# Optimization experiments

Hardware: AMD Instinct MI355X
Metric: run time of the kernel (lower is better)

## Reference

```python
import jax, jax.numpy as jnp
import numpy as np

EPS = 1e-5

def _ln(x, g, b):
    mu = jnp.mean(x, axis=-1, keepdims=True)
    var = jnp.mean((x - mu) ** 2, axis=-1, keepdims=True)
    return (x - mu) * jax.lax.rsqrt(var + EPS) * g + b

def setup_inputs() -> dict:
    key = jax.random.key(0)
    B, V, I, H = 32, 48, 24, 768
    ks = jax.random.split(key, 10)
    s = 0.02
    return {
        'variables': jax.random.normal(ks[0], (B, V, H), jnp.float32),
        'interventions': jax.random.normal(ks[1], (B, I, H), jnp.float32),
        # variable_encoder: Linear(H,H) + LayerNorm(H)
        'W_enc': jax.random.normal(ks[2], (H, H), jnp.float32) * s,
        'b_enc': jnp.zeros((H,), jnp.float32),
        'g_enc': jnp.ones((H,), jnp.float32),
        'be_enc': jnp.zeros((H,), jnp.float32),
        # graph_generator: Linear(2H,H) + LN(H) + ReLU + Linear(H,1) + Sigmoid
        'Wg1': jax.random.normal(ks[3], (2 * H, H), jnp.float32) * s,
        'bg1': jnp.zeros((H,), jnp.float32),
        'g_g': jnp.ones((H,), jnp.float32),
        'b_g': jnp.zeros((H,), jnp.float32),
        'Wg2': jax.random.normal(ks[4], (H, 1), jnp.float32) * s,
        'bg2': jnp.zeros((1,), jnp.float32),
        # intervention_predictor: Linear(2H,H) + LN(H) + ReLU + Linear(H,H)
        'Wi1': jax.random.normal(ks[5], (2 * H, H), jnp.float32) * s,
        'bi1': jnp.zeros((H,), jnp.float32),
        'g_i': jnp.ones((H,), jnp.float32),
        'b_i': jnp.zeros((H,), jnp.float32),
        'Wi2': jax.random.normal(ks[6], (H, H), jnp.float32) * s,
        'bi2': jnp.zeros((H,), jnp.float32),
    }

def reference(variables, interventions, W_enc, b_enc, g_enc, be_enc,
              Wg1, bg1, g_g, b_g, Wg2, bg2, Wi1, bi1, g_i, b_i, Wi2, bi2):
    H = variables.shape[-1]
    V = variables.shape[1]
    # variable encoder: Linear + LayerNorm + ReLU
    enc = jax.nn.relu(_ln(variables @ W_enc + b_enc, g_enc, be_enc))  # [B,V,H]

    # graph generator over all ordered pairs (i,j): concat([enc_i, enc_j]) @ Wg1
    # split Wg1 so the concat-matmul becomes two small GEMMs + broadcast add
    hi = jnp.einsum('bvh,hk->bvk', enc, Wg1[:H])   # contribution of enc_i
    hj = jnp.einsum('bvh,hk->bvk', enc, Wg1[H:])   # contribution of enc_j
    h = jax.nn.relu(_ln(hi[:, :, None, :] + hj[:, None, :, :] + bg1, g_g, b_g))  # [B,V,V,H]
    score = jax.nn.sigmoid(jnp.squeeze(h @ Wg2, -1) + bg2[0])  # [B,V,V]
    # diagonal (i==j) is never written in the original -> stays zero
    causal_graph = score * (1.0 - jnp.eye(V, dtype=score.dtype))

    # intervention predictor: concat([intervention_i, enc_j]) -> MLP
    ha = jnp.einsum('bih,hk->bik', interventions, Wi1[:H])  # [B,I,H]
    hb = jnp.einsum('bvh,hk->bvk', enc, Wi1[H:])            # [B,V,H]
    h2 = jax.nn.relu(_ln(ha[:, :, None, :] + hb[:, None, :, :] + bi1, g_i, b_i))  # [B,I,V,H]
    effects = h2 @ Wi2 + bi2  # [B,I,V,H]

    return (effects, causal_graph, enc)
```

## Files before the change

### kernel.cpp

```cpp
#include <hip/hip_runtime.h>
#include <math.h>

#define Bp 32
#define Vp 48
#define Ip 24
#define Hp 768
#define EPS 1e-5f

#define EFFECTS_SIZE (Bp*Ip*Vp*Hp)
#define GRAPH_SIZE   (Bp*Vp*Vp)
#define ENC_SIZE     (Bp*Vp*Hp)
#define MS           (Hp*Hp)

typedef __attribute__((ext_vector_type(8))) short short8;
typedef __attribute__((ext_vector_type(4))) float floatx4;
typedef __attribute__((ext_vector_type(2))) float floatx2;
typedef __attribute__((ext_vector_type(2))) unsigned int uintx2;
typedef __attribute__((ext_vector_type(4))) unsigned int uintx4;

__device__ __forceinline__ unsigned short f2bf(float f) {
    unsigned int u = __float_as_uint(f);
    u += 0x7fffu + ((u >> 16) & 1u);
    return (unsigned short)(u >> 16);
}
__device__ __forceinline__ unsigned int f2bf2(float a, float b) {
    return (unsigned int)f2bf(a) | ((unsigned int)f2bf(b) << 16);
}

__device__ __forceinline__ uintx4 ln8(floatx4 xa, floatx4 xb, float mu, float rs,
                                      floatx4 ga, floatx4 gb, floatx4 ba, floatx4 bb)
{
    float y0 = fmaxf((xa.x - mu) * rs * ga.x + ba.x, 0.f);
    float y1 = fmaxf((xa.y - mu) * rs * ga.y + ba.y, 0.f);
    float y2 = fmaxf((xa.z - mu) * rs * ga.z + ba.z, 0.f);
    float y3 = fmaxf((xa.w - mu) * rs * ga.w + ba.w, 0.f);
    float y4 = fmaxf((xb.x - mu) * rs * gb.x + bb.x, 0.f);
    float y5 = fmaxf((xb.y - mu) * rs * gb.y + bb.y, 0.f);
    float y6 = fmaxf((xb.z - mu) * rs * gb.z + bb.z, 0.f);
    float y7 = fmaxf((xb.w - mu) * rs * gb.w + bb.w, 0.f);
    uintx4 v;
    v.x = f2bf2(y0, y1); v.y = f2bf2(y2, y3);
    v.z = f2bf2(y4, y5); v.w = f2bf2(y6, y7);
    return v;
}

__global__ __launch_bounds__(256) void pack_weights(
    const float* __restrict__ W_enc, const float* __restrict__ Wg1,
    const float* __restrict__ Wi1, const float* __restrict__ Wi2,
    unsigned short* __restrict__ packed)
{
    const int bid = blockIdx.x;
    const int m = bid / 288;
    const int rem = bid - m * 288;
    const int T = rem / 6;
    const int u = rem - T * 6;
    const float* src;
    switch (m) {
        case 0: src = W_enc; break;
        case 1: src = Wg1; break;
        case 2: src = Wg1 + Hp * Hp; break;
        case 3: src = Wi1 + Hp * Hp; break;
        case 4: src = Wi1; break;
        default: src = Wi2; break;
    }
    unsigned short* dst = packed + (size_t)m * MS;
    const int lane = threadIdx.x & 63;
    const int kq = threadIdx.x >> 6;
    const int col = T * 16 + (lane & 15);
    const int krow0 = (lane >> 4) * 8;
    const int kb = kq + 4 * u;
    unsigned int w[4];
#pragma unroll
    for (int p2 = 0; p2 < 4; ++p2) {
        float f0 = src[(size_t)(kb * 32 + krow0 + 2 * p2)     * Hp + col];
        float f1 = src[(size_t)(kb * 32 + krow0 + 2 * p2 + 1) * Hp + col];
        w[p2] = f2bf2(f0, f1);
    }
    uintx4 v; v.x = w[0]; v.y = w[1]; v.z = w[2]; v.w = w[3];
    *(uintx4*)(dst + ((size_t)(T * 24 + kb) * 64 + lane) * 8) = v;
}

__global__ __launch_bounds__(256) void convert_inputs(
    const float* __restrict__ vars, const float* __restrict__ intv,
    const float* __restrict__ bg1, const float* __restrict__ bi1,
    unsigned short* __restrict__ varb, unsigned short* __restrict__ intvb,
    float* __restrict__ bias2304)
{
    const int p = blockIdx.x * 256 + threadIdx.x;
    const int VPn = ENC_SIZE / 2;
    if (p < VPn) {
        float2 f = ((const float2*)vars)[p];
        ((unsigned int*)varb)[p] = f2bf2(f.x, f.y);
    } else {
        int q = p - VPn;
        float2 f = ((const float2*)intv)[q];
        ((unsigned int*)intvb)[q] = f2bf2(f.x, f.y);
    }
    if (blockIdx.x == 0) {
        for (int t = threadIdx.x; t < 2304; t += 256)
            bias2304[t] = (t < 768) ? 0.0f : (t < 1536 ? bg1[t - 768] : bi1[t - 1536]);
    }
}

__global__ __launch_bounds__(256) void gemm32(
    const unsigned short* __restrict__ A, const unsigned short* __restrict__ Bpk,
    const float* __restrict__ bias, float* __restrict__ C, int ldc)
{
    __shared__ unsigned short Asl[2 * 24 * 64 * 8];
    const int tid = threadIdx.x, wave = tid >> 6, lane = tid & 63;
    const int m0 = blockIdx.x * 32;

#pragma unroll
    for (int uu = 0; uu < 12; ++uu) {
        const int s = tid + 256 * uu;
        const int mt = s / 1536;
        const int r2 = s - mt * 1536;
        const int kb = r2 >> 6;
        const int L  = r2 & 63;
        uintx4 v = *(const uintx4*)(A + (size_t)(m0 + mt * 16 + (L & 15)) * Hp
                                      + kb * 32 + (L >> 4) * 8);
        *(uintx4*)(&Asl[((mt * 24 + kb) * 64 + (L ^ (kb & 7))) * 8]) = v;
    }
    __syncthreads();

    const int mrow = lane & 15, kq = lane >> 4;
    const int rot = ((blockIdx.x * 5 + blockIdx.y) & 7) * 3;
    const int wavep = (wave + blockIdx.x) & 3;
    const int Tg0 = blockIdx.y * 12 + wavep * 3;
    const unsigned short* Bbase = Bpk + (size_t)Tg0 * 12288 + lane * 8;

    const floatx4 z = {0.f, 0.f, 0.f, 0.f};
    floatx4 acc[2][3];
#pragma unroll
    for (int mt = 0; mt < 2; ++mt)
#pragma unroll
        for (int nt = 0; nt < 3; ++nt) acc[mt][nt] = z;

    short8 bbuf[4][3], abuf[2][2];
#pragma unroll
    for (int d = 0; d < 3; ++d) {
        int kc = d + rot; if (kc >= 24) kc -= 24;
#pragma unroll
        for (int nt = 0; nt < 3; ++nt)
            bbuf[d][nt] = *(const short8*)(Bbase + (size_t)nt * 12288 + kc * 512);
    }
    {
        int kc = rot;
#pragma unroll
        for (int mt = 0; mt < 2; ++mt)
            abuf[0][mt] = *(const short8*)(&Asl[((mt * 24 + kc) * 64 + (lane ^ (kc & 7))) * 8]);
    }

#pragma unroll
    for (int kb = 0; kb < 24; ++kb) {
        if (kb + 3 < 24) {
            int kc = kb + 3 + rot; if (kc >= 24) kc -= 24;
#pragma unroll
            for (int nt = 0; nt < 3; ++nt)
                bbuf[(kb + 3) & 3][nt] =
                    *(const short8*)(Bbase + (size_t)nt * 12288 + kc * 512);
        }
        if (kb + 1 < 24) {
            int kc = kb + 1 + rot; if (kc >= 24) kc -= 24;
#pragma unroll
            for (int mt = 0; mt < 2; ++mt)
                abuf[(kb + 1) & 1][mt] = *(const short8*)(
                    &Asl[((mt * 24 + kc) * 64 + (lane ^ (kc & 7))) * 8]);
        }
        __builtin_amdgcn_s_setprio(1);
#pragma unroll
        for (int mt = 0; mt < 2; ++mt)
#pragma unroll
            for (int nt = 0; nt < 3; ++nt)
                acc[mt][nt] = __builtin_amdgcn_mfma_f32_16x16x32_bf16(
                    abuf[kb & 1][mt], bbuf[kb & 3][nt], acc[mt][nt], 0, 0, 0);
        __builtin_amdgcn_s_setprio(0);
    }

#pragma unroll
    for (int nt = 0; nt < 3; ++nt) {
        const int colg = (Tg0 + nt) * 16 + mrow;
        const float bv = bias ? bias[colg] : 0.0f;
#pragma unroll
        for (int mt = 0; mt < 2; ++mt)
#pragma unroll
            for (int r = 0; r < 4; ++r)
                C[(size_t)(m0 + mt * 16 + kq * 4 + r) * ldc + colg] = acc[mt][nt][r] + bv;
    }
}

__global__ __launch_bounds__(256) void gemm_ln(
    const unsigned short* __restrict__ A, const unsigned short* __restrict__ Bpk,
    const float* __restrict__ bias, const float* __restrict__ g,
    const float* __restrict__ be, float* __restrict__ encf,
    unsigned short* __restrict__ encb)
{
    __shared__ unsigned short Asl[24 * 64 * 8];
    __shared__ float Cl[16 * 772];
    const int tid = threadIdx.x, wave = tid >> 6, lane = tid & 63;
    const int m0 = blockIdx.x * 16;

#pragma unroll
    for (int uu = 0; uu < 6; ++uu) {
        const int s = tid + 256 * uu;
        const int kb = s >> 6, L = s & 63;
        uintx4 v = *(const uintx4*)(A + (size_t)(m0 + (L & 15)) * Hp
                                      + kb * 32 + (L >> 4) * 8);
        *(uintx4*)(&Asl[(kb * 64 + (L ^ (kb & 7))) * 8]) = v;
    }
    __syncthreads();

    const int mrow = lane & 15, kq = lane >> 4;
    const floatx4 z = {0.f, 0.f, 0.f, 0.f};
#pragma unroll
    for (int G = 0; G < 2; ++G) {
        const int Tg0 = G * 24 + wave * 6;
        const unsigned short* Bbase = Bpk + (size_t)Tg0 * 12288 + lane * 8;
        floatx4 acc[6];
#pragma unroll
        for (int nt = 0; nt < 6; ++nt) acc[nt] = z;
        short8 bbuf[4][6], abuf[2];
#pragma unroll
        for (int d = 0; d < 3; ++d)
#pragma unroll
            for (int nt = 0; nt < 6; ++nt)
                bbuf[d][nt] = *(const short8*)(Bbase + (size_t)nt * 12288 + d * 512);
        abuf[0] = *(const short8*)(&Asl[(0 * 64 + (lane ^ 0)) * 8]);

#pragma unroll
        for (int kb = 0; kb < 24; ++kb) {
            if (kb + 3 < 24) {
                const int kc = kb + 3;
#pragma unroll
                for (int nt = 0; nt < 6; ++nt)
                    bbuf[(kb + 3) & 3][nt] =
                        *(const short8*)(Bbase + (size_t)nt * 12288 + kc * 512);
            }
            if (kb + 1 < 24) {
                const int kc = kb + 1;
                abuf[(kb + 1) & 1] = *(const short8*)(
                    &Asl[(kc * 64 + (lane ^ (kc & 7))) * 8]);
            }
            __builtin_amdgcn_s_setprio(1);
#pragma unroll
            for (int nt = 0; nt < 6; ++nt)
                acc[nt] = __builtin_amdgcn_mfma_f32_16x16x32_bf16(
                    abuf[kb & 1], bbuf[kb & 3][nt], acc[nt], 0, 0, 0);
            __builtin_amdgcn_s_setprio(0);
        }

#pragma unroll
        for (int nt = 0; nt < 6; ++nt) {
            const int colg = (Tg0 + nt) * 16 + mrow;
            const float bv = bias[colg];
#pragma unroll
            for (int r = 0; r < 4; ++r)
                Cl[(kq * 4 + r) * 772 + colg] = acc[nt][r] + bv;
        }
    }
    __syncthreads();

    floatx4 gv[3], bev[3];
#pragma unroll
    for (int t = 0; t < 3; ++t) {
        gv[t]  = ((const floatx4*)g)[lane + 64 * t];
        bev[t] = ((const floatx4*)be)[lane + 64 * t];
    }
#pragma unroll
    for (int rr = 0; rr < 4; ++rr) {
        const int row = wave * 4 + rr;
        const floatx4* cp = (const floatx4*)(Cl + row * 772);
        floatx4 x[3]; float s = 0.f, q = 0.f;
#pragma unroll
        for (int t = 0; t < 3; ++t) {
            x[t] = cp[lane + 64 * t];
            s += x[t].x + x[t].y + x[t].z + x[t].w;
            q += x[t].x*x[t].x + x[t].y*x[t].y + x[t].z*x[t].z + x[t].w*x[t].w;
        }
#pragma unroll
        for (int m = 1; m < 64; m <<= 1) { s += __shfl_xor(s, m, 64); q += __shfl_xor(q, m, 64); }
        const float mu = s * (1.0f / Hp);
        const float rs = rsqrtf(q * (1.0f / Hp) - mu * mu + EPS);
        floatx4* of = (floatx4*)(encf + (size_t)(m0 + row) * Hp);
        uintx2* ob = (uintx2*)(encb + (size_t)(m0 + row) * Hp);
#pragma unroll
        for (int t = 0; t < 3; ++t) {
            floatx4 y;
            y.x = fmaxf((x[t].x - mu) * rs * gv[t].x + bev[t].x, 0.f);
            y.y = fmaxf((x[t].y - mu) * rs * gv[t].y + bev[t].y, 0.f);
            y.z = fmaxf((x[t].z - mu) * rs * gv[t].z + bev[t].z, 0.f);
            y.w = fmaxf((x[t].w - mu) * rs * gv[t].w + bev[t].w, 0.f);
            __builtin_nontemporal_store(y, &of[lane + 64 * t]);
            uintx2 p; p.x = f2bf2(y.x, y.y); p.y = f2bf2(y.z, y.w);
            ob[lane + 64 * t] = p;
        }
    }
}

__global__ __launch_bounds__(256) void graph_kernel(
    const float* __restrict__ ws2, const float* __restrict__ gg_,
    const float* __restrict__ bb_, const float* __restrict__ Wg2,
    const float* __restrict__ bg2, float* __restrict__ out)
{
    const int wave = threadIdx.x >> 6, lane = threadIdx.x & 63;
    const int p = blockIdx.x;
    const int b = p / Vp, i = p - b * Vp;
    const floatx4* hi4 = (const floatx4*)(ws2 + (size_t)p * 2304);
    const floatx4* gg4 = (const floatx4*)gg_;
    const floatx4* bb4 = (const floatx4*)bb_;
    const floatx4* w24 = (const floatx4*)Wg2;
    floatx4 ri[3], gg[3], bb[3], w2[3];
#pragma unroll
    for (int c = 0; c < 3; ++c) {
        const int k = lane + 64 * c;
        ri[c] = hi4[k]; gg[c] = gg4[k]; bb[c] = bb4[k]; w2[c] = w24[k];
    }
    const float bg2v = bg2[0];
    const int j0 = wave * 12;
    for (int jj = 0; jj < 12; jj += 2) {
        const int jA = j0 + jj, jB = jA + 1;
        const floatx4* hjA = (const floatx4*)(ws2 + (size_t)(b * Vp + jA) * 2304 + 768);
        const floatx4* hjB = (const floatx4*)(ws2 + (size_t)(b * Vp + jB) * 2304 + 768);
        floatx4 xA[3], xB[3];
        float sA = 0.f, qA = 0.f, sB = 0.f, qB = 0.f;
#pragma unroll
        for (int c = 0; c < 3; ++c) {
            const int k = lane + 64 * c;
            xA[c] = ri[c] + hjA[k];
            xB[c] = ri[c] + hjB[k];
            sA += xA[c].x + xA[c].y + xA[c].z + xA[c].w;
            qA += xA[c].x * xA[c].x + xA[c].y * xA[c].y + xA[c].z * xA[c].z + xA[c].w * xA[c].w;
            sB += xB[c].x + xB[c].y + xB[c].z + xB[c].w;
            qB += xB[c].x * xB[c].x + xB[c].y * xB[c].y + xB[c].z * xB[c].z + xB[c].w * xB[c].w;
        }
#pragma unroll
        for (int m = 1; m < 64; m <<= 1) {
            sA += __shfl_xor(sA, m, 64); qA += __shfl_xor(qA, m, 64);
            sB += __shfl_xor(sB, m, 64); qB += __shfl_xor(qB, m, 64);
        }
        const float muA = sA * (1.0f / Hp);
        const float rsA = rsqrtf(qA * (1.0f / Hp) - muA * muA + EPS);
        const float muB = sB * (1.0f / Hp);
        const float rsB = rsqrtf(qB * (1.0f / Hp) - muB * muB + EPS);
        float pdA = 0.f, pdB = 0.f;
#pragma unroll
        for (int c = 0; c < 3; ++c) {
            float yA0 = fmaxf((xA[c].x - muA) * rsA * gg[c].x + bb[c].x, 0.f);
            float yA1 = fmaxf((xA[c].y - muA) * rsA * gg[c].y + bb[c].y, 0.f);
            float yA2 = fmaxf((xA[c].z - muA) * rsA * gg[c].z + bb[c].z, 0.f);
            float yA3 = fmaxf((xA[c].w - muA) * rsA * gg[c].w + bb[c].w, 0.f);
            pdA = fmaf(yA0, w2[c].x, pdA); pdA = fmaf(yA1, w2[c].y, pdA);
            pdA = fmaf(yA2, w2[c].z, pdA); pdA = fmaf(yA3, w2[c].w, pdA);
            float yB0 = fmaxf((xB[c].x - muB) * rsB * gg[c].x + bb[c].x, 0.f);
            float yB1 = fmaxf((xB[c].y - muB) * rsB * gg[c].y + bb[c].y, 0.f);
            float yB2 = fmaxf((xB[c].z - muB) * rsB * gg[c].z + bb[c].z, 0.f);
            float yB3 = fmaxf((xB[c].w - muB) * rsB * gg[c].w + bb[c].w, 0.f);
            pdB = fmaf(yB0, w2[c].x, pdB); pdB = fmaf(yB1, w2[c].y, pdB);
            pdB = fmaf(yB2, w2[c].z, pdB); pdB = fmaf(yB3, w2[c].w, pdB);
        }
#pragma unroll
        for (int m = 1; m < 64; m <<= 1) {
            pdA += __shfl_xor(pdA, m, 64);
            pdB += __shfl_xor(pdB, m, 64);
        }
        if (lane == 0) {
            float scA = (i == jA) ? 0.0f : 1.0f / (1.0f + expf(-(pdA + bg2v)));
            float scB = (i == jB) ? 0.0f : 1.0f / (1.0f + expf(-(pdB + bg2v)));
            out[(size_t)p * Vp + jA] = scA;
            out[(size_t)p * Vp + jB] = scB;
        }
    }
}

__global__ __launch_bounds__(512, 2) void effects96(
    const float* __restrict__ ha, const float* __restrict__ ws2,
    const float* __restrict__ g_i, const float* __restrict__ b_i,
    const unsigned short* __restrict__ Bpk, const float* __restrict__ bi2,
    float* __restrict__ out)
{
    __shared__ unsigned short Asl[6 * 24 * 64 * 8];
    const int tid = threadIdx.x, wave = tid >> 6, lane = tid & 63;
    const int bid = blockIdx.x;
    const int pair = bid >> 1, nhalf = bid & 1;
    const int b = pair / 12;
    const int bi0 = b * Ip + (pair - b * 12) * 2;
    const int half = lane >> 5, hl = lane & 31;

    {
        const floatx4* ha0 = (const floatx4*)(ha + (size_t)bi0 * Hp);
        const floatx4* ha1 = (const floatx4*)(ha + (size_t)(bi0 + 1) * Hp);
        const floatx4* gp = (const floatx4*)g_i;
        const floatx4* bp = (const floatx4*)b_i;
        floatx4 hv0[6], hv1[6], gv[6], bv[6];
#pragma unroll
        for (int t = 0; t < 3; ++t) {
            hv0[2*t] = ha0[2*hl + 64*t];  hv0[2*t+1] = ha0[2*hl + 1 + 64*t];
            hv1[2*t] = ha1[2*hl + 64*t];  hv1[2*t+1] = ha1[2*hl + 1 + 64*t];
            gv[2*t]  = gp[2*hl + 64*t];   gv[2*t+1]  = gp[2*hl + 1 + 64*t];
            bv[2*t]  = bp[2*hl + 64*t];   bv[2*t+1]  = bp[2*hl + 1 + 64*t];
        }

#pragma unroll
        for (int p = 0; p < 3; ++p) {
            const int j = wave * 6 + 2 * p + half;
            const floatx4* hbp = (const floatx4*)(ws2 + (size_t)(b * Vp + j) * 2304 + 1536);
            floatx4 x0[6], x1[6];
            float s0 = 0.f, q0 = 0.f, s1 = 0.f, q1 = 0.f;
#pragma unroll
            for (int t = 0; t < 3; ++t) {
                const floatx4 hA = hbp[2*hl + 64*t];
                const floatx4 hB = hbp[2*hl + 1 + 64*t];
                x0[2*t]   = hv0[2*t]   + hA;  x0[2*t+1] = hv0[2*t+1] + hB;
                x1[2*t]   = hv1[2*t]   + hA;  x1[2*t+1] = hv1[2*t+1] + hB;
            }
#pragma unroll
            for (int c = 0; c < 6; ++c) {
                s0 += x0[c].x + x0[c].y + x0[c].z + x0[c].w;
                q0 += x0[c].x*x0[c].x + x0[c].y*x0[c].y + x0[c].z*x0[c].z + x0[c].w*x0[c].w;
                s1 += x1[c].x + x1[c].y + x1[c].z + x1[c].w;
                q1 += x1[c].x*x1[c].x + x1[c].y*x1[c].y + x1[c].z*x1[c].z + x1[c].w*x1[c].w;
            }
#pragma unroll
            for (int m = 1; m < 32; m <<= 1) {
                s0 += __shfl_xor(s0, m, 64); q0 += __shfl_xor(q0, m, 64);
                s1 += __shfl_xor(s1, m, 64); q1 += __shfl_xor(q1, m, 64);
            }
            const float mu0 = s0 * (1.0f / Hp);
            const float rs0 = rsqrtf(q0 * (1.0f / Hp) - mu0 * mu0 + EPS);
            const float mu1 = s1 * (1.0f / Hp);
            const float rs1 = rsqrtf(q1 * (1.0f / Hp) - mu1 * mu1 + EPS);
            const int mt0 = j >> 4, mt1 = 3 + mt0, mr = j & 15;
#pragma unroll
            for (int t = 0; t < 3; ++t) {
                const int cpk = hl + 32 * t;
                const int kb = cpk >> 2, kq2 = cpk & 3;
                const int swz = (kq2 * 16 + mr) ^ (kb & 7);
                uintx4 v0 = ln8(x0[2*t], x0[2*t+1], mu0, rs0,
                                gv[2*t], gv[2*t+1], bv[2*t], bv[2*t+1]);
                *(uintx4*)(&Asl[((mt0 * 24 + kb) * 64 + swz) * 8]) = v0;
                uintx4 v1 = ln8(x1[2*t], x1[2*t+1], mu1, rs1,
                                gv[2*t], gv[2*t+1], bv[2*t], bv[2*t+1]);
                *(uintx4*)(&Asl[((mt1 * 24 + kb) * 64 + swz) * 8]) = v1;
            }
        }
    }
    __syncthreads();

    const int mrow = lane & 15, kq = lane >> 4;
    const int rot = (pair & 7) * 3;
    const int wavep = (wave + pair) & 7;
    const int Tg0 = nhalf * 24 + wavep * 3;
    const unsigned short* Bbase = Bpk + (size_t)Tg0 * 12288 + lane * 8;

    const floatx4 z = {0.f, 0.f, 0.f, 0.f};
    floatx4 acc[6][3];
#pragma unroll
    for (int mt = 0; mt < 6; ++mt)
#pragma unroll
        for (int nt = 0; nt < 3; ++nt) acc[mt][nt] = z;

    short8 bbuf[4][3], abuf[2][6];
#pragma unroll
    for (int d = 0; d < 3; ++d) {
        int kc = d + rot; if (kc >= 24) kc -= 24;
#pragma unroll
        for (int nt = 0; nt < 3; ++nt)
            bbuf[d][nt] = *(const short8*)(Bbase + (size_t)nt * 12288 + kc * 512);
    }
    {
        int kc = rot;
#pragma unroll
        for (int mt = 0; mt < 6; ++mt)
            abuf[0][mt] = *(const short8*)(&Asl[((mt * 24 + kc) * 64 + (lane ^ (kc & 7))) * 8]);
    }

#pragma unroll
    for (int kb = 0; kb < 24; ++kb) {
        if (kb + 3 < 24) {
            int kc = kb + 3 + rot; if (kc >= 24) kc -= 24;
#pragma unroll
            for (int nt = 0; nt < 3; ++nt)
                bbuf[(kb + 3) & 3][nt] =
                    *(const short8*)(Bbase + (size_t)nt * 12288 + kc * 512);
        }
        if (kb + 1 < 24) {
            int kc = kb + 1 + rot; if (kc >= 24) kc -= 24;
#pragma unroll
            for (int mt = 0; mt < 6; ++mt)
                abuf[(kb + 1) & 1][mt] = *(const short8*)(
                    &Asl[((mt * 24 + kc) * 64 + (lane ^ (kc & 7))) * 8]);
        }
        __builtin_amdgcn_s_setprio(1);
#pragma unroll
        for (int mt = 0; mt < 6; ++mt)
#pragma unroll
            for (int nt = 0; nt < 3; ++nt)
                acc[mt][nt] = __builtin_amdgcn_mfma_f32_16x16x32_bf16(
                    abuf[kb & 1][mt], bbuf[kb & 3][nt], acc[mt][nt], 0, 0, 0);
        __builtin_amdgcn_s_setprio(0);
    }

#pragma unroll
    for (int nt = 0; nt < 3; ++nt) {
        const int colg = (Tg0 + nt) * 16 + mrow;
        const float biasv = bi2[colg];
#pragma unroll
        for (int mt = 0; mt < 6; ++mt) {
#pragma unroll
            for (int r = 0; r < 4; ++r) {
                const int rr = mt * 16 + kq * 4 + r;
                __builtin_nontemporal_store(
                    acc[mt][nt][r] + biasv,
                    &out[(size_t)(bi0 * 48 + rr) * Hp + colg]);
            }
        }
    }
}

extern "C" void kernel_launch(void* const* d_in, const int* in_sizes, int n_in,
                              void* d_out, int out_size, void* d_ws, size_t ws_size,
                              hipStream_t stream) {
    const float* variables     = (const float*)d_in[0];
    const float* interventions = (const float*)d_in[1];
    const float* W_enc  = (const float*)d_in[2];
    const float* b_enc  = (const float*)d_in[3];
    const float* g_enc  = (const float*)d_in[4];
    const float* be_enc = (const float*)d_in[5];
    const float* Wg1 = (const float*)d_in[6];
    const float* bg1 = (const float*)d_in[7];
    const float* g_g = (const float*)d_in[8];
    const float* b_g = (const float*)d_in[9];
    const float* Wg2 = (const float*)d_in[10];
    const float* bg2 = (const float*)d_in[11];
    const float* Wi1 = (const float*)d_in[12];
    const float* bi1 = (const float*)d_in[13];
    const float* g_i = (const float*)d_in[14];
    const float* b_i = (const float*)d_in[15];
    const float* Wi2 = (const float*)d_in[16];
    const float* bi2 = (const float*)d_in[17];

    float* out = (float*)d_out;
    float* effects = out;
    float* graph = out + EFFECTS_SIZE;
    float* enc_f = out + EFFECTS_SIZE + GRAPH_SIZE;

    char* wsb = (char*)d_ws;
    unsigned short* packedW = (unsigned short*)wsb;
    float* ws2  = (float*)(wsb + 7077888);
    float* ha   = (float*)(wsb + 7077888 + 14155776);
    unsigned short* varb  = (unsigned short*)(wsb + 23592960);
    unsigned short* intvb = (unsigned short*)(wsb + 25952256);
    unsigned short* encb  = (unsigned short*)(wsb + 27131904);
    float* bias2304 = (float*)(wsb + 29491200);

    pack_weights<<<1728, 256, 0, stream>>>(W_enc, Wg1, Wi1, Wi2, packedW);
    convert_inputs<<<3456, 256, 0, stream>>>(variables, interventions, bg1, bi1,
                                             varb, intvb, bias2304);
    gemm_ln<<<96, 256, 0, stream>>>(varb, packedW, b_enc, g_enc, be_enc,
                                    enc_f, encb);
    gemm32<<<dim3(48, 12), 256, 0, stream>>>(encb, packedW + (size_t)1 * MS,
                                             bias2304, ws2, 2304);
    gemm32<<<dim3(24, 4), 256, 0, stream>>>(intvb, packedW + (size_t)4 * MS,
                                            nullptr, ha, Hp);
    graph_kernel<<<Bp * Vp, 256, 0, stream>>>(ws2, g_g, b_g, Wg2, bg2, graph);
    effects96<<<768, 512, 0, stream>>>(ha, ws2, g_i, b_i,
                                       packedW + (size_t)5 * MS, bi2, effects);
}
```

Before: 280.7 us.

## Merge ws2/ha GEMMs into one launch and stage effects output through LDS

Combines the two gemm32 launches into a single grid, where the extra y-rows handle the intervention projection, saving one kernel launch and its tail. In the effects kernel, accumulator results are now written to shared memory and then stored to global memory as coalesced 16-byte nontemporal vector stores instead of scattered scalar stores. The staging adds two barriers and relies on the reused A tile buffer being large enough for a 96x384 float tile.

Result: no change. 280.2 us (-0.2%).

```diff
diff --git a/kernel.cpp b/kernel.cpp
--- a/kernel.cpp
+++ b/kernel.cpp
@@ -102,13 +102,14 @@
     }
 }
 
-__global__ __launch_bounds__(256) void gemm32(
+__device__ __forceinline__ void gemm32_body(
+    unsigned short* Asl,
     const unsigned short* __restrict__ A, const unsigned short* __restrict__ Bpk,
-    const float* __restrict__ bias, float* __restrict__ C, int ldc)
-{
-    __shared__ unsigned short Asl[2 * 24 * 64 * 8];
+    const float* __restrict__ bias, float* __restrict__ C, int ldc,
+    int bx, int by)
+{
     const int tid = threadIdx.x, wave = tid >> 6, lane = tid & 63;
-    const int m0 = blockIdx.x * 32;
+    const int m0 = bx * 32;
 
 #pragma unroll
     for (int uu = 0; uu < 12; ++uu) {
@@ -124,9 +125,9 @@
     __syncthreads();
 
     const int mrow = lane & 15, kq = lane >> 4;
-    const int rot = ((blockIdx.x * 5 + blockIdx.y) & 7) * 3;
-    const int wavep = (wave + blockIdx.x) & 3;
-    const int Tg0 = blockIdx.y * 12 + wavep * 3;
+    const int rot = ((bx * 5 + by) & 7) * 3;
+    const int wavep = (wave + bx) & 3;
+    const int Tg0 = by * 12 + wavep * 3;
     const unsigned short* Bbase = Bpk + (size_t)Tg0 * 12288 + lane * 8;
 
     const floatx4 z = {0.f, 0.f, 0.f, 0.f};
@@ -186,6 +187,21 @@
 #pragma unroll
             for (int r = 0; r < 4; ++r)
                 C[(size_t)(m0 + mt * 16 + kq * 4 + r) * ldc + colg] = acc[mt][nt][r] + bv;
+    }
+}
+
+__global__ __launch_bounds__(256) void gemm_ws2_ha(
+    const unsigned short* __restrict__ A1, const unsigned short* __restrict__ B1,
+    const float* __restrict__ bias1, float* __restrict__ C1,
+    const unsigned short* __restrict__ A2, const unsigned short* __restrict__ B2,
+    float* __restrict__ C2)
+{
+    __shared__ unsigned short Asl[2 * 24 * 64 * 8];
+    if (blockIdx.y < 12) {
+        gemm32_body(Asl, A1, B1, bias1, C1, 2304, blockIdx.x, blockIdx.y);
+    } else {
+        const int idx = (blockIdx.y - 12) * 48 + blockIdx.x;
+        gemm32_body(Asl, A2, B2, nullptr, C2, Hp, idx % 24, idx / 24);
     }
 }
 
@@ -500,19 +516,32 @@
         __builtin_amdgcn_s_setprio(0);
     }
 
+    __syncthreads();
+    float* F = (float*)Asl;
 #pragma unroll
     for (int nt = 0; nt < 3; ++nt) {
         const int colg = (Tg0 + nt) * 16 + mrow;
+        const int coll = colg - nhalf * 384;
         const float biasv = bi2[colg];
 #pragma unroll
         for (int mt = 0; mt < 6; ++mt) {
 #pragma unroll
             for (int r = 0; r < 4; ++r) {
                 const int rr = mt * 16 + kq * 4 + r;
-                __builtin_nontemporal_store(
-                    acc[mt][nt][r] + biasv,
-                    &out[(size_t)(bi0 * 48 + rr) * Hp + colg]);
-            }
+                F[rr * 384 + coll] = acc[mt][nt][r] + biasv;
+            }
+        }
+    }
+    __syncthreads();
+    {
+        const floatx4* F4 = (const floatx4*)F;
+        float* obase = out + (size_t)(bi0 * 48) * Hp + nhalf * 384;
+#pragma unroll
+        for (int u = 0; u < 18; ++u) {
+            const int idx = tid + 512 * u;
+            const int row = idx / 96, c4 = idx - row * 96;
+            floatx4 v = F4[row * 96 + c4];
+            __builtin_nontemporal_store(v, (floatx4*)(obase + (size_t)row * Hp) + c4);
         }
     }
 }
@@ -558,10 +587,9 @@
                                              varb, intvb, bias2304);
     gemm_ln<<<96, 256, 0, stream>>>(varb, packedW, b_enc, g_enc, be_enc,
                                     enc_f, encb);
-    gemm32<<<dim3(48, 12), 256, 0, stream>>>(encb, packedW + (size_t)1 * MS,
-                                             bias2304, ws2, 2304);
-    gemm32<<<dim3(24, 4), 256, 0, stream>>>(intvb, packedW + (size_t)4 * MS,
-                                            nullptr, ha, Hp);
+    gemm_ws2_ha<<<dim3(48, 14), 256, 0, stream>>>(
+        encb, packedW + (size_t)1 * MS, bias2304, ws2,
+        intvb, packedW + (size_t)4 * MS, ha);
     graph_kernel<<<Bp * Vp, 256, 0, stream>>>(ws2, g_g, b_g, Wg2, bg2, graph);
     effects96<<<768, 512, 0, stream>>>(ha, ws2, g_i, b_i,
                                        packedW + (size_t)5 * MS, bi2, effects);
```
